# Kernel optimization log

Hardware: AMD Instinct MI355X
Metric: run time of the kernel (lower is better)

## Reference

```python
import jax, jax.numpy as jnp
import numpy as np

B, C, H, W = 2, 256, 64, 64
NH = 4          # num_heads -> ch = C // NH = 64
G = 32          # GroupNorm groups (normalization(channels))
EPS = 1e-5


def setup_inputs() -> dict:
    key = jax.random.key(0)
    ks = jax.random.split(key, 7)
    s = 1.0 / np.sqrt(C).astype(np.float32)
    return {
        "x": jax.random.normal(ks[0], (B, C, H, W), jnp.float32),
        "gn_scale": 1.0 + 0.02 * jax.random.normal(ks[1], (C,), jnp.float32),
        "gn_bias": 0.02 * jax.random.normal(ks[2], (C,), jnp.float32),
        "w_qkv": s * jax.random.normal(ks[3], (3 * C, C), jnp.float32),
        "b_qkv": jnp.zeros((3 * C,), jnp.float32),
        # NOTE: original zero-inits proj_out; we use random weights so the
        # attention path contributes to the output (meaningful baseline).
        "w_proj": s * jax.random.normal(ks[4], (C, C), jnp.float32),
        "b_proj": jnp.zeros((C,), jnp.float32),
    }


def reference(x, gn_scale, gn_bias, w_qkv, b_qkv, w_proj, b_proj):
    b, c = x.shape[0], x.shape[1]
    spatial = x.shape[2:]
    t = int(np.prod(spatial))
    xf = x.reshape(b, c, t)                      # [B, C, T]

    # GroupNorm(32) over (channels-in-group, T)
    xg = xf.reshape(b, G, c // G, t)
    mu = xg.mean(axis=(2, 3), keepdims=True)
    var = xg.var(axis=(2, 3), keepdims=True)
    xn = ((xg - mu) * jax.lax.rsqrt(var + EPS)).reshape(b, c, t)
    xn = xn * gn_scale[None, :, None] + gn_bias[None, :, None]

    # 1x1 conv -> qkv: [B, 3C, T]
    qkv = jnp.einsum('oc,bct->bot', w_qkv, xn) + b_qkv[None, :, None]

    # QKVAttentionLegacy: reshape (B*H, 3*ch, T) then split
    ch = c // NH
    qkv_h = qkv.reshape(b * NH, 3 * ch, t)
    q, k, v = jnp.split(qkv_h, 3, axis=1)        # each [B*H, ch, T]
    scale = 1.0 / np.sqrt(np.sqrt(ch)).astype(np.float32)
    w = jnp.einsum('bct,bcs->bts', q * scale, k * scale)   # [B*H, T, T]
    w = jax.nn.softmax(w.astype(jnp.float32), axis=-1).astype(qkv.dtype)
    a = jnp.einsum('bts,bcs->bct', w, v).reshape(b, c, t)  # [B, C, T]

    # proj 1x1 conv + residual
    h = jnp.einsum('oc,bct->bot', w_proj, a) + b_proj[None, :, None]
    return (xf + h).reshape(b, c, *spatial)
```

## Files before the change

kernel.cpp:

```cpp
#include <hip/hip_runtime.h>
#include <math.h>

#define T 4096
#define C 256
#define BATCH 2
#define NH 4
#define G 32
#define CPG 8
#define EPS 1e-5f
#define LOG2E 1.4426950408889634f
#define QSCALE (0.125f * LOG2E)
#define KSPLIT 4
#define KRANGE (T / KSPLIT)
#define BH (BATCH * NH)

typedef __attribute__((ext_vector_type(8))) short bfv8;
typedef __attribute__((ext_vector_type(4))) short bfv4;
typedef __attribute__((ext_vector_type(4))) float f32x4;

static __device__ __forceinline__ short f2bf(float f) {
    union { float f; unsigned u; } v; v.f = f;
    return (short)((v.u + 0x7FFFu + ((v.u >> 16) & 1u)) >> 16);
}
static __device__ __forceinline__ short f2bf_fast(float f) {
    union { float f; unsigned u; } v; v.f = f;
    return (short)((v.u + 0x8000u) >> 16);
}
static __device__ __forceinline__ float bf2f(short s) {
    union { float f; unsigned u; } v; v.u = ((unsigned)(unsigned short)s) << 16;
    return v.f;
}

#if __has_builtin(__builtin_amdgcn_exp2f)
#define EXP2(x) __builtin_amdgcn_exp2f(x)
#else
#define EXP2(x) exp2f(x)
#endif

#define MFMA16(a, b, c) __builtin_amdgcn_mfma_f32_16x16x16bf16_1k(a, b, c, 0, 0, 0)

#define AS1 __attribute__((address_space(1)))
#define AS3 __attribute__((address_space(3)))
static __device__ __forceinline__ void gll16(const void* g, void* l) {
    __builtin_amdgcn_global_load_lds((const AS1 void*)g, (AS3 void*)l, 16, 0, 0);
}

__global__ __launch_bounds__(256) void prep_w(const float* __restrict__ wq,
                                              const float* __restrict__ wp,
                                              short* __restrict__ wqb,
                                              short* __restrict__ wpb) {
    int i = blockIdx.x * 256 + threadIdx.x;
    const int NQ = 768 * 256 / 4;
    float4 v; short* dst;
    if (i < NQ) { v = ((const float4*)wq)[i]; dst = wqb + i * 4; }
    else        { int j = i - NQ; v = ((const float4*)wp)[j]; dst = wpb + j * 4; }
    bfv4 o = { f2bf(v.x), f2bf(v.y), f2bf(v.z), f2bf(v.w) };
    *(bfv4*)dst = o;
}

__global__ __launch_bounds__(256) void gn_stats(const float* __restrict__ x,
                                                float* __restrict__ gnp) {
    const int blk = blockIdx.x;
    const int ts  = blockIdx.y;
    const int b = blk / G, g = blk % G;
    const float* xp = x + ((size_t)b * C + g * CPG) * T + ts * 1024;

    const int tid = threadIdx.x;
    float s = 0.f, ss = 0.f;
    #pragma unroll
    for (int u = 0; u < CPG; u++) {
        float4 v = ((const float4*)(xp + (size_t)u * T))[tid];
        s  += v.x + v.y + v.z + v.w;
        ss += v.x*v.x + v.y*v.y + v.z*v.z + v.w*v.w;
    }
    __shared__ float rs[256], rss[256];
    rs[tid] = s; rss[tid] = ss;
    __syncthreads();
    for (int off = 128; off > 0; off >>= 1) {
        if (tid < off) { rs[tid] += rs[tid+off]; rss[tid] += rss[tid+off]; }
        __syncthreads();
    }
    if (tid == 0) {
        gnp[(blk * 4 + ts) * 2 + 0] = rs[0];
        gnp[(blk * 4 + ts) * 2 + 1] = rss[0];
    }
}

__global__ __launch_bounds__(256) void gn_norm(const float* __restrict__ x,
                                               const float* __restrict__ scale,
                                               const float* __restrict__ bias,
                                               const float* __restrict__ gnp,
                                               short* __restrict__ xnT) {
    const int blk = blockIdx.x;
    const int ts  = blockIdx.y;
    const int b = blk / G, g = blk % G;
    const int c0 = g * CPG;
    const float* xp = x + ((size_t)b * C + c0) * T;

    float s = 0.f, ss = 0.f;
    #pragma unroll
    for (int i = 0; i < 4; i++) {
        s  += gnp[(blk * 4 + i) * 2 + 0];
        ss += gnp[(blk * 4 + i) * 2 + 1];
    }
    const float inv_n = 1.0f / (CPG * T);
    const float mu  = s * inv_n;
    const float var = ss * inv_n - mu * mu;
    const float rstd = rsqrtf(var + EPS);

    float sc[CPG], bi[CPG];
    #pragma unroll
    for (int u = 0; u < CPG; u++) {
        sc[u] = scale[c0+u] * rstd;
        bi[u] = bias[c0+u] - mu * sc[u];
    }

    const int t = ts * 1024 + threadIdx.x * 4;
    float vv[CPG][4];
    #pragma unroll
    for (int u = 0; u < CPG; u++) {
        float4 v = *(const float4*)&xp[(size_t)u * T + t];
        vv[u][0] = v.x * sc[u] + bi[u];
        vv[u][1] = v.y * sc[u] + bi[u];
        vv[u][2] = v.z * sc[u] + bi[u];
        vv[u][3] = v.w * sc[u] + bi[u];
    }
    #pragma unroll
    for (int j = 0; j < 4; j++) {
        bfv8 w = { f2bf(vv[0][j]), f2bf(vv[1][j]), f2bf(vv[2][j]), f2bf(vv[3][j]),
                   f2bf(vv[4][j]), f2bf(vv[5][j]), f2bf(vv[6][j]), f2bf(vv[7][j]) };
        *(bfv8*)&xnT[((size_t)b * T + t + j) * C + c0] = w;
    }
}

__global__ __launch_bounds__(256) void gemm_qkv(
    const short* __restrict__ wq,
    const float* __restrict__ bq,
    const short* __restrict__ xnT,
    short* __restrict__ qb, short* __restrict__ kb, short* __restrict__ vb)
{
    const int b  = blockIdx.z;
    const int t0 = blockIdx.x * 64;
    const int ot = blockIdx.y;
    const int h = ot / 3, part = ot % 3;
    const int o0 = ot * 64;

    __shared__ short sm[8192];
    short* Ab = sm;
    short* Bb = sm + 4096;

    const int tid = threadIdx.x, lane = tid & 63, wave = tid >> 6;
    const int col = lane & 15, quad = lane >> 4;
    const short* xb = xnT + (size_t)b * T * C;

    f32x4 acc[4];
    #pragma unroll
    for (int g = 0; g < 4; g++) { acc[g][0]=0.f; acc[g][1]=0.f; acc[g][2]=0.f; acc[g][3]=0.f; }

    for (int k0 = 0; k0 < C; k0 += 64) {
        __syncthreads();
        #pragma unroll
        for (int hh = 0; hh < 2; hh++) {
            gll16(wq + (size_t)(o0 + 16*wave + col) * C + k0 + hh*32 + quad*8,
                  Ab + (hh*4 + wave) * 512);
            gll16(xb + (size_t)(t0 + 16*wave + col) * C + k0 + hh*32 + quad*8,
                  Bb + (hh*4 + wave) * 512);
        }
        __syncthreads();
        #pragma unroll
        for (int hh = 0; hh < 2; hh++) {
            bfv8 af = *(const bfv8*)(Ab + (hh*4 + wave) * 512 + lane*8);
            #pragma unroll
            for (int g = 0; g < 4; g++) {
                bfv8 bf = *(const bfv8*)(Bb + (hh*4 + g) * 512 + lane*8);
                acc[g] = __builtin_amdgcn_mfma_f32_16x16x32_bf16(af, bf, acc[g], 0, 0, 0);
            }
        }
    }

    const int olocal = 16*wave + quad*4;
    float bias_r[4];
    #pragma unroll
    for (int r = 0; r < 4; r++) bias_r[r] = bq[o0 + olocal + r];
    const size_t hd = (size_t)(b * NH + h);

    if (part < 2) {
        short* dst = (part == 0 ? qb : kb) + hd * T * 64;
        const float sc = (part == 0) ? QSCALE : 1.0f;
        #pragma unroll
        for (int g = 0; g < 4; g++) {
            int t = t0 + 16*g + col;
            bfv4 w = { f2bf((acc[g][0] + bias_r[0]) * sc),
                       f2bf((acc[g][1] + bias_r[1]) * sc),
                       f2bf((acc[g][2] + bias_r[2]) * sc),
                       f2bf((acc[g][3] + bias_r[3]) * sc) };
            *(bfv4*)&dst[(size_t)t * 64 + olocal] = w;
        }
    } else {
        short* dst = vb + hd * 64 * T;
        #pragma unroll
        for (int g = 0; g < 4; g++)
            #pragma unroll
            for (int r = 0; r < 4; r++)
                dst[(size_t)(olocal + r) * T + t0 + 16*g + col] =
                    f2bf(acc[g][r] + bias_r[r]);
    }
}

__global__ __launch_bounds__(256) void attn_kernel(
    const short* __restrict__ qb,
    const short* __restrict__ kb,
    const short* __restrict__ vb,
    short* __restrict__ opart,
    float* __restrict__ lp)
{
    __shared__ short smem[16384];
    const int bh = blockIdx.y;
    const int ks = blockIdx.z;
    const int t0 = blockIdx.x * 64;
    const int k0base = ks * KRANGE;
    const short* kbh = kb + (size_t)bh * T * 64;
    const short* vbh = vb + (size_t)bh * 64 * T;

    const int tid  = threadIdx.x;
    const int lane = tid & 63;
    const int wave = tid >> 6;
    const int col  = lane & 15;
    const int quad = lane >> 4;

    const short* qrow = qb + (size_t)bh * T * 64 + (size_t)(t0 + wave*16 + col) * 64;
    bfv8 qf0 = *(const bfv8*)(qrow + quad*8);
    bfv8 qf1 = *(const bfv8*)(qrow + 32 + quad*8);

    f32x4 oacc[4];
    #pragma unroll
    for (int g = 0; g < 4; g++) { oacc[g][0]=0.f; oacc[g][1]=0.f; oacc[g][2]=0.f; oacc[g][3]=0.f; }
    float lsum = 0.f;

    const int vq = ((quad >> 1) * 16 + col) * 8 + (quad & 1) * 4;

    #define STAGE_KV(buf, s0)                                                  \
        {                                                                      \
            short* base = smem + (buf) * 8192;                                 \
            _Pragma("unroll")                                                  \
            for (int u = 0; u < 2; u++) {                                      \
                gll16(kbh + (size_t)((s0) + 16*wave + col) * 64 + (quad + 4*u)*8, \
                      base + (wave + 4*u) * 512);                              \
                gll16(vbh + (size_t)(16*wave + col) * T + (s0) + (quad + 4*u)*8, \
                      base + 4096 + (wave + 4*u) * 512);                       \
            }                                                                  \
        }

    STAGE_KV(0, k0base)

    for (int it = 0; it < KRANGE/64; it++) {
        __syncthreads();
        if (it + 1 < KRANGE/64) STAGE_KV((it+1) & 1, k0base + (it+1)*64)

        const short* kvb = smem + (it & 1) * 8192;

        f32x4 s[4];
        #pragma unroll
        for (int g = 0; g < 4; g++) {
            bfv8 kf0 = *(const bfv8*)(kvb + g*512 + lane*8);
            bfv8 kf1 = *(const bfv8*)(kvb + (4+g)*512 + lane*8);
            f32x4 a0 = {0.f, 0.f, 0.f, 0.f};
            a0 = __builtin_amdgcn_mfma_f32_16x16x32_bf16(kf0, qf0, a0, 0, 0, 0);
            a0 = __builtin_amdgcn_mfma_f32_16x16x32_bf16(kf1, qf1, a0, 0, 0, 0);
            s[g] = a0;
        }

        bfv4 pf[4];
        #pragma unroll
        for (int g = 0; g < 4; g++)
            #pragma unroll
            for (int r = 0; r < 4; r++) {
                float p = EXP2(s[g][r]);
                lsum += p;
                pf[g][r] = f2bf_fast(p);
            }

        const short* vbase = kvb + 4096;
        #pragma unroll
        for (int g = 0; g < 4; g++) {
            bfv4 v0 = *(const bfv4*)(vbase + g*512 + vq);
            bfv4 v1 = *(const bfv4*)(vbase + g*512 + vq + 256);
            bfv4 v2 = *(const bfv4*)(vbase + (4+g)*512 + vq);
            bfv4 v3 = *(const bfv4*)(vbase + (4+g)*512 + vq + 256);
            oacc[g] = MFMA16(v0, pf[0], oacc[g]);
            oacc[g] = MFMA16(v1, pf[1], oacc[g]);
            oacc[g] = MFMA16(v2, pf[2], oacc[g]);
            oacc[g] = MFMA16(v3, pf[3], oacc[g]);
        }
    }

    lsum += __shfl_xor(lsum, 16);
    lsum += __shfl_xor(lsum, 32);

    const size_t rowbase = (size_t)(ks*BH + bh) * T + t0 + wave*16;
    short* opb = opart + (rowbase + col) * 64;
    #pragma unroll
    for (int g = 0; g < 4; g++) {
        bfv4 w = { f2bf(oacc[g][0]), f2bf(oacc[g][1]),
                   f2bf(oacc[g][2]), f2bf(oacc[g][3]) };
        *(bfv4*)(opb + 16*g + quad*4) = w;
    }
    if (lane < 16)
        lp[rowbase + col] = lsum;
}

__global__ __launch_bounds__(256) void gemm_proj(
    const short* __restrict__ wp,
    const float* __restrict__ bp,
    const short* __restrict__ opart,
    const float* __restrict__ lp,
    const float* __restrict__ x,
    float* __restrict__ out)
{
    const int b  = blockIdx.z;
    const int t0 = blockIdx.x * 64;
    const int o0 = blockIdx.y * 64;

    __shared__ short sm[8192];
    short* Ab = sm;
    short* Bb = sm + 4096;

    const int tid = threadIdx.x, lane = tid & 63, wave = tid >> 6;
    const int col = lane & 15, quad = lane >> 4;

    const int trow = t0 + 16*wave + col;
    float rl4[NH];
    #pragma unroll
    for (int hh = 0; hh < NH; hh++) {
        float ls = 0.f;
        #pragma unroll
        for (int ks = 0; ks < KSPLIT; ks++)
            ls += lp[((size_t)(ks*BH) + b*NH + hh) * T + trow];
        rl4[hh] = 1.0f / ls;
    }

    f32x4 acc[4];
    #pragma unroll
    for (int g = 0; g < 4; g++) { acc[g][0]=0.f; acc[g][1]=0.f; acc[g][2]=0.f; acc[g][3]=0.f; }

    for (int k0 = 0; k0 < C; k0 += 64) {
        __syncthreads();
        #pragma unroll
        for (int hh = 0; hh < 2; hh++) {
            gll16(wp + (size_t)(o0 + 16*wave + col) * C + k0 + hh*32 + quad*8,
                  Ab + (hh*4 + wave) * 512);
            const int chg = k0 + hh*32 + quad*8;
            const int hd = chg >> 6, chin = chg & 63;
            const short* ob = opart + (((size_t)(b*NH + hd)) * T + trow) * 64 + chin;
            float a8[8] = {0.f,0.f,0.f,0.f,0.f,0.f,0.f,0.f};
            #pragma unroll
            for (int ks = 0; ks < KSPLIT; ks++) {
                bfv8 v = *(const bfv8*)(ob + (size_t)ks * BH * T * 64);
                #pragma unroll
                for (int u = 0; u < 8; u++) a8[u] += bf2f(v[u]);
            }
            const float rl = rl4[hd];
            bfv8 pk;
            #pragma unroll
            for (int u = 0; u < 8; u++) pk[u] = f2bf(a8[u] * rl);
            *(bfv8*)(Bb + (hh*4 + wave) * 512 + lane*8) = pk;
        }
        __syncthreads();
        #pragma unroll
        for (int hh = 0; hh < 2; hh++) {
            bfv8 af = *(const bfv8*)(Ab + (hh*4 + wave) * 512 + lane*8);
            #pragma unroll
            for (int g = 0; g < 4; g++) {
                bfv8 bf = *(const bfv8*)(Bb + (hh*4 + g) * 512 + lane*8);
                acc[g] = __builtin_amdgcn_mfma_f32_16x16x32_bf16(af, bf, acc[g], 0, 0, 0);
            }
        }
    }

    const int olocal = 16*wave + quad*4;
    #pragma unroll
    for (int r = 0; r < 4; r++) {
        const int o = o0 + olocal + r;
        const float bias = bp[o];
        const size_t rowoff = ((size_t)b * C + o) * T;
        #pragma unroll
        for (int g = 0; g < 4; g++) {
            const size_t idx = rowoff + t0 + 16*g + col;
            out[idx] = acc[g][r] + bias + x[idx];
        }
    }
}

extern "C" void kernel_launch(void* const* d_in, const int* in_sizes, int n_in,
                              void* d_out, int out_size, void* d_ws, size_t ws_size,
                              hipStream_t stream) {
    (void)in_sizes; (void)n_in; (void)out_size; (void)ws_size;
    const float* x        = (const float*)d_in[0];
    const float* gn_scale = (const float*)d_in[1];
    const float* gn_bias  = (const float*)d_in[2];
    const float* w_qkv    = (const float*)d_in[3];
    const float* b_qkv    = (const float*)d_in[4];
    const float* w_proj   = (const float*)d_in[5];
    const float* b_proj   = (const float*)d_in[6];
    float* out = (float*)d_out;

    short* ws    = (short*)d_ws;
    short* qb    = ws;
    short* kb    = qb  + (size_t)BH * T * 64;
    short* vb    = kb  + (size_t)BH * T * 64;
    short* xnT   = vb  + (size_t)BH * T * 64;
    short* wqb   = xnT + (size_t)BATCH * T * C;
    short* wpb   = wqb + 768 * 256;
    short* opart = wpb + 256 * 256;
    float* lp    = (float*)(opart + (size_t)KSPLIT * BH * T * 64);
    float* gnp   = lp + (size_t)KSPLIT * BH * T;

    prep_w<<<dim3(256), 256, 0, stream>>>(w_qkv, w_proj, wqb, wpb);
    gn_stats<<<dim3(BATCH * G, 4), 256, 0, stream>>>(x, gnp);
    gn_norm<<<dim3(BATCH * G, 4), 256, 0, stream>>>(x, gn_scale, gn_bias, gnp, xnT);
    gemm_qkv<<<dim3(T/64, 12, BATCH), 256, 0, stream>>>(wqb, b_qkv, xnT, qb, kb, vb);
    attn_kernel<<<dim3(T/64, BH, KSPLIT), 256, 0, stream>>>(qb, kb, vb, opart, lp);
    gemm_proj<<<dim3(T/64, 4, BATCH), 256, 0, stream>>>(wpb, b_proj, opart, lp, x, out);
}
```

Before: 174.6 us.

## Process two query tiles per attention block to reuse staged K/V tiles

```diff
diff --git a/kernel.cpp b/kernel.cpp
--- a/kernel.cpp
+++ b/kernel.cpp
@@ -217,7 +217,7 @@
     __shared__ short smem[16384];
     const int bh = blockIdx.y;
     const int ks = blockIdx.z;
-    const int t0 = blockIdx.x * 64;
+    const int t0 = blockIdx.x * 128;
     const int k0base = ks * KRANGE;
     const short* kbh = kb + (size_t)bh * T * 64;
     const short* vbh = vb + (size_t)bh * 64 * T;
@@ -228,14 +228,20 @@
     const int col  = lane & 15;
     const int quad = lane >> 4;
 
-    const short* qrow = qb + (size_t)bh * T * 64 + (size_t)(t0 + wave*16 + col) * 64;
-    bfv8 qf0 = *(const bfv8*)(qrow + quad*8);
-    bfv8 qf1 = *(const bfv8*)(qrow + 32 + quad*8);
-
-    f32x4 oacc[4];
-    #pragma unroll
-    for (int g = 0; g < 4; g++) { oacc[g][0]=0.f; oacc[g][1]=0.f; oacc[g][2]=0.f; oacc[g][3]=0.f; }
-    float lsum = 0.f;
+    const short* qrowA = qb + (size_t)bh * T * 64 + (size_t)(t0 + wave*16 + col) * 64;
+    const short* qrowB = qrowA + (size_t)64 * 64;
+    bfv8 qfA0 = *(const bfv8*)(qrowA + quad*8);
+    bfv8 qfA1 = *(const bfv8*)(qrowA + 32 + quad*8);
+    bfv8 qfB0 = *(const bfv8*)(qrowB + quad*8);
+    bfv8 qfB1 = *(const bfv8*)(qrowB + 32 + quad*8);
+
+    f32x4 oaccA[4], oaccB[4];
+    #pragma unroll
+    for (int g = 0; g < 4; g++) {
+        oaccA[g][0]=0.f; oaccA[g][1]=0.f; oaccA[g][2]=0.f; oaccA[g][3]=0.f;
+        oaccB[g][0]=0.f; oaccB[g][1]=0.f; oaccB[g][2]=0.f; oaccB[g][3]=0.f;
+    }
+    float lsumA = 0.f, lsumB = 0.f;
 
     const int vq = ((quad >> 1) * 16 + col) * 8 + (quad & 1) * 4;
 
@@ -259,26 +265,31 @@
 
         const short* kvb = smem + (it & 1) * 8192;
 
-        f32x4 s[4];
+        bfv4 pfA[4], pfB[4];
         #pragma unroll
         for (int g = 0; g < 4; g++) {
             bfv8 kf0 = *(const bfv8*)(kvb + g*512 + lane*8);
             bfv8 kf1 = *(const bfv8*)(kvb + (4+g)*512 + lane*8);
-            f32x4 a0 = {0.f, 0.f, 0.f, 0.f};
-            a0 = __builtin_amdgcn_mfma_f32_16x16x32_bf16(kf0, qf0, a0, 0, 0, 0);
-            a0 = __builtin_amdgcn_mfma_f32_16x16x32_bf16(kf1, qf1, a0, 0, 0, 0);
-            s[g] = a0;
-        }
-
-        bfv4 pf[4];
-        #pragma unroll
-        for (int g = 0; g < 4; g++)
+            f32x4 a;
+            a[0]=0.f; a[1]=0.f; a[2]=0.f; a[3]=0.f;
+            a = __builtin_amdgcn_mfma_f32_16x16x32_bf16(kf0, qfA0, a, 0, 0, 0);
+            a = __builtin_amdgcn_mfma_f32_16x16x32_bf16(kf1, qfA1, a, 0, 0, 0);
             #pragma unroll
             for (int r = 0; r < 4; r++) {
-                float p = EXP2(s[g][r]);
-                lsum += p;
-                pf[g][r] = f2bf_fast(p);
+                float p = EXP2(a[r]);
+                lsumA += p;
+                pfA[g][r] = f2bf_fast(p);
             }
+            a[0]=0.f; a[1]=0.f; a[2]=0.f; a[3]=0.f;
+            a = __builtin_amdgcn_mfma_f32_16x16x32_bf16(kf0, qfB0, a, 0, 0, 0);
+            a = __builtin_amdgcn_mfma_f32_16x16x32_bf16(kf1, qfB1, a, 0, 0, 0);
+            #pragma unroll
+            for (int r = 0; r < 4; r++) {
+                float p = EXP2(a[r]);
+                lsumB += p;
+                pfB[g][r] = f2bf_fast(p);
+            }
+        }
 
         const short* vbase = kvb + 4096;
         #pragma unroll
@@ -287,26 +298,39 @@
             bfv4 v1 = *(const bfv4*)(vbase + g*512 + vq + 256);
             bfv4 v2 = *(const bfv4*)(vbase + (4+g)*512 + vq);
             bfv4 v3 = *(const bfv4*)(vbase + (4+g)*512 + vq + 256);
-            oacc[g] = MFMA16(v0, pf[0], oacc[g]);
-            oacc[g] = MFMA16(v1, pf[1], oacc[g]);
-            oacc[g] = MFMA16(v2, pf[2], oacc[g]);
-            oacc[g] = MFMA16(v3, pf[3], oacc[g]);
-        }
-    }
-
-    lsum += __shfl_xor(lsum, 16);
-    lsum += __shfl_xor(lsum, 32);
-
-    const size_t rowbase = (size_t)(ks*BH + bh) * T + t0 + wave*16;
-    short* opb = opart + (rowbase + col) * 64;
+            oaccA[g] = MFMA16(v0, pfA[0], oaccA[g]);
+            oaccB[g] = MFMA16(v0, pfB[0], oaccB[g]);
+            oaccA[g] = MFMA16(v1, pfA[1], oaccA[g]);
+            oaccB[g] = MFMA16(v1, pfB[1], oaccB[g]);
+            oaccA[g] = MFMA16(v2, pfA[2], oaccA[g]);
+            oaccB[g] = MFMA16(v2, pfB[2], oaccB[g]);
+            oaccA[g] = MFMA16(v3, pfA[3], oaccA[g]);
+            oaccB[g] = MFMA16(v3, pfB[3], oaccB[g]);
+        }
+    }
+
+    lsumA += __shfl_xor(lsumA, 16);
+    lsumA += __shfl_xor(lsumA, 32);
+    lsumB += __shfl_xor(lsumB, 16);
+    lsumB += __shfl_xor(lsumB, 32);
+
+    const size_t rowbaseA = (size_t)(ks*BH + bh) * T + t0 + wave*16;
+    const size_t rowbaseB = rowbaseA + 64;
+    short* opbA = opart + (rowbaseA + col) * 64;
+    short* opbB = opart + (rowbaseB + col) * 64;
     #pragma unroll
     for (int g = 0; g < 4; g++) {
-        bfv4 w = { f2bf(oacc[g][0]), f2bf(oacc[g][1]),
-                   f2bf(oacc[g][2]), f2bf(oacc[g][3]) };
-        *(bfv4*)(opb + 16*g + quad*4) = w;
-    }
-    if (lane < 16)
-        lp[rowbase + col] = lsum;
+        bfv4 wA = { f2bf(oaccA[g][0]), f2bf(oaccA[g][1]),
+                    f2bf(oaccA[g][2]), f2bf(oaccA[g][3]) };
+        *(bfv4*)(opbA + 16*g + quad*4) = wA;
+        bfv4 wB = { f2bf(oaccB[g][0]), f2bf(oaccB[g][1]),
+                    f2bf(oaccB[g][2]), f2bf(oaccB[g][3]) };
+        *(bfv4*)(opbB + 16*g + quad*4) = wB;
+    }
+    if (lane < 16) {
+        lp[rowbaseA + col] = lsumA;
+        lp[rowbaseB + col] = lsumB;
+    }
 }
 
 __global__ __launch_bounds__(256) void gemm_proj(
@@ -419,6 +443,6 @@
     gn_stats<<<dim3(BATCH * G, 4), 256, 0, stream>>>(x, gnp);
     gn_norm<<<dim3(BATCH * G, 4), 256, 0, stream>>>(x, gn_scale, gn_bias, gnp, xnT);
     gemm_qkv<<<dim3(T/64, 12, BATCH), 256, 0, stream>>>(wqb, b_qkv, xnT, qb, kb, vb);
-    attn_kernel<<<dim3(T/64, BH, KSPLIT), 256, 0, stream>>>(qb, kb, vb, opart, lp);
+    attn_kernel<<<dim3(T/128, BH, KSPLIT), 256, 0, stream>>>(qb, kb, vb, opart, lp);
     gemm_proj<<<dim3(T/64, 4, BATCH), 256, 0, stream>>>(wpb, b_proj, opart, lp, x, out);
 }
```

New measurement: 157.3 us. 1.11x faster.
